# Performance work log

Measured on AMD Instinct MI355X. Metric: run time of the kernel, lower is better.

Reference implementation:

```python
import jax, jax.numpy as jnp
import numpy as np

Nx, Nh, Ny = 512, 512, 2
T, B = 64, 256

def setup_inputs() -> dict:
    key = jax.random.key(0)
    ks = jax.random.split(key, 7)
    x = jax.random.normal(ks[0], (T, B, Nx), dtype=jnp.float32)
    # parameters per random_weight_init([Nx, Nh, Ny], bias=True) + extra W[2]
    w1 = jax.random.normal(ks[1], (Nh, Nx), dtype=jnp.float32) / np.sqrt(Nx)
    b1 = jax.random.normal(ks[2], (Nh, 1), dtype=jnp.float32)
    w2 = (jax.random.normal(ks[3], (Ny, Nh), dtype=jnp.float32) / np.sqrt(Nh)).T  # [Nh, Ny]
    b2 = jax.random.normal(ks[4], (Ny,), dtype=jnp.float32)
    w21 = jax.random.normal(ks[5], (Nh, Ny), dtype=jnp.float32) / np.sqrt(Ny)
    lam = jnp.float32(0.99)
    eta = jnp.float32(-5.0 / Nx)
    return {"x": x, "w1": w1, "b1": b1, "w2": w2, "b2": b2,
            "w21": w21, "lam": lam, "eta": eta}


def reference(x, w1, b1, w2, b2, w21, lam, eta):
    # x: [T, B, Nx]
    lam_c = jnp.minimum(lam, 1.0)  # lam clamped to max=1.0 each forward
    b1v = b1[:, 0]                 # [Nh]

    def step(carry, xt):
        A, a2 = carry              # A: [B, Nh, Nx], a2: [B, Ny]
        # a1 = b1 + (w1 + A) @ x + w21 @ a2
        a1 = (b1v
              + jnp.einsum('hx,bx->bh', w1, xt)
              + jnp.einsum('bhx,bx->bh', A, xt)
              + jnp.einsum('hy,by->bh', w21, a2))
        h = jax.nn.sigmoid(a1)     # [B, Nh]
        # Hebbian fast-weight update: A = lam*A + eta * outer(h, x)
        A_new = lam_c * A + eta * h[:, :, None] * xt[:, None, :]
        a2_new = b2 + h @ w2       # [B, Ny]
        y = jax.nn.sigmoid(a2_new)
        return (A_new, a2_new), (h, y)

    A0 = jnp.zeros((x.shape[1], w1.shape[0], w1.shape[1]), dtype=x.dtype)
    a20 = jnp.zeros((x.shape[1], w2.shape[1]), dtype=x.dtype)
    _, (hiddens, outputs) = jax.lax.scan(step, (A0, a20), x)
    # match torch shapes: hiddens [T, B, Nh, 1], outputs [T, B, Ny]
    return hiddens[..., None], outputs
```

## Files before the change

kernel.cpp:

```cpp
#include <hip/hip_runtime.h>
#include <hip/hip_bf16.h>
#include <math.h>

#define T_STEPS 64
#define BATCH   256
#define NX      512
#define NH      512

typedef short bf16x8 __attribute__((ext_vector_type(8)));
typedef float f32x4  __attribute__((ext_vector_type(4)));

__device__ __forceinline__ float dpp_sum64(float v) {
    v += __int_as_float(__builtin_amdgcn_update_dpp(0, __float_as_int(v), 0x111, 0xf, 0xf, true));
    v += __int_as_float(__builtin_amdgcn_update_dpp(0, __float_as_int(v), 0x112, 0xf, 0xf, true));
    v += __int_as_float(__builtin_amdgcn_update_dpp(0, __float_as_int(v), 0x114, 0xf, 0xf, true));
    v += __int_as_float(__builtin_amdgcn_update_dpp(0, __float_as_int(v), 0x118, 0xf, 0xf, true));
    v += __int_as_float(__builtin_amdgcn_update_dpp(0, __float_as_int(v), 0x142, 0xf, 0xf, true));
    v += __int_as_float(__builtin_amdgcn_update_dpp(0, __float_as_int(v), 0x143, 0xf, 0xf, true));
    return v;
}

__device__ __forceinline__ __hip_bfloat162 cvt2(float a, float b) {
    return __float22bfloat162_rn(make_float2(a, b));
}

__global__ __launch_bounds__(256) void w1_prep_kernel(
    const float* __restrict__ w1, unsigned short* __restrict__ w1f)
{
    int tid = blockIdx.x * 256 + threadIdx.x;
    int row = tid >> 6;
    int oct = tid & 63;
    const float* s = &w1[(size_t)row * 512 + oct * 8];
    float4 v0 = *(const float4*)s;
    float4 v1 = *(const float4*)(s + 4);
    union { __hip_bfloat162 q[4]; int4 pk; } u;
    u.q[0] = cvt2(v0.x, v0.y); u.q[1] = cvt2(v0.z, v0.w);
    u.q[2] = cvt2(v1.x, v1.y); u.q[3] = cvt2(v1.z, v1.w);
    int g = ((oct >> 2) * 32 + (row >> 4)) * 64 + (row & 15) + 16 * (oct & 3);
    *(int4*)&w1f[(size_t)g * 8] = u.pk;
}

__global__ __launch_bounds__(512, 1) void fused_kernel(
    const float* __restrict__ x,
    const unsigned short* __restrict__ w1f,
    const float* __restrict__ b1,
    const float* __restrict__ w2,
    const float* __restrict__ b2,
    const float* __restrict__ w21,
    const float* __restrict__ lamp,
    const float* __restrict__ etap,
    float* __restrict__ outH,
    float* __restrict__ outY)
{
    const int b    = blockIdx.x;
    const int h    = threadIdx.x;
    const int lane = h & 63;
    const int wv   = h >> 6;

    __shared__ float Hs[64][512];
    __shared__ float Gl[64][66];
    __shared__ float C[16][64];
    __shared__ float lam_pow[64];
    __shared__ float red[2][16];

    unsigned short* xs = (unsigned short*)&Hs[0][0];

    const float eta = etap[0];
    const float lam = fminf(lamp[0], 1.0f);
    const float2 w21v = *(const float2*)&w21[2 * h];
    const float2 w2v  = *(const float2*)&w2[2 * h];
    const float b20 = b2[0], b21 = b2[1];
    float* oHb = outH + (size_t)b * NH + h;

    if (h < 64)
        lam_pow[h] = (h == 0) ? 1.0f : exp2f((float)h * log2f(lam));
#pragma unroll
    for (int i = 0; i < 8; ++i) {
        int r = wv + i * 8;
        int o = lane;
        const float* src = &x[((size_t)r * BATCH + b) * NX + o * 8];
        float4 v0 = *(const float4*)src;
        float4 v1 = *(const float4*)(src + 4);
        union { __hip_bfloat162 q[4]; int4 pk; } u;
        u.q[0] = cvt2(v0.x, v0.y); u.q[1] = cvt2(v0.z, v0.w);
        u.q[2] = cvt2(v1.x, v1.y); u.q[3] = cvt2(v1.z, v1.w);
        int g = ((o >> 2) * 4 + (r >> 4)) * 64 + (r & 15) + 16 * (o & 3);
        *(int4*)&xs[g * 8] = u.pk;
    }
    __syncthreads();

    bf16x8 bfp[2][4];
#pragma unroll
    for (int nf = 0; nf < 4; ++nf)
        bfp[0][nf] = *(const bf16x8*)&w1f[(size_t)((wv * 4 + nf) * 64 + lane) * 8];

    {
        const int mt_g = wv >> 1;
#pragma unroll
        for (int j = 0; j < 2; ++j) {
            const int nt_g = (wv & 1) * 2 + j;
            f32x4 gacc = {};
#pragma unroll
            for (int ks = 0; ks < 16; ++ks) {
                bf16x8 afr = *(const bf16x8*)&xs[((ks * 4 + mt_g) * 64 + lane) * 8];
                bf16x8 bfr = *(const bf16x8*)&xs[((ks * 4 + nt_g) * 64 + lane) * 8];
                gacc = __builtin_amdgcn_mfma_f32_16x16x32_bf16(afr, bfr, gacc, 0, 0, 0);
            }
#pragma unroll
            for (int r = 0; r < 4; ++r)
                Gl[mt_g * 16 + ((lane >> 4) << 2) + r][nt_g * 16 + (lane & 15)] = gacc[r];
        }
    }

    {
        f32x4 pacc[4][4] = {};
#pragma unroll
        for (int ks = 0; ks < 16; ++ks) {
            if (ks < 15) {
#pragma unroll
                for (int nf = 0; nf < 4; ++nf)
                    bfp[(ks + 1) & 1][nf] = *(const bf16x8*)
                        &w1f[(size_t)(((ks + 1) * 32 + wv * 4 + nf) * 64 + lane) * 8];
            }
            bf16x8 afr[4];
#pragma unroll
            for (int mt = 0; mt < 4; ++mt)
                afr[mt] = *(const bf16x8*)&xs[((ks * 4 + mt) * 64 + lane) * 8];
#pragma unroll
            for (int mt = 0; mt < 4; ++mt)
#pragma unroll
                for (int nf = 0; nf < 4; ++nf)
                    pacc[mt][nf] = __builtin_amdgcn_mfma_f32_16x16x32_bf16(
                        afr[mt], bfp[ks & 1][nf], pacc[mt][nf], 0, 0, 0);
        }

        __syncthreads();

        float bc[4];
#pragma unroll
        for (int nf = 0; nf < 4; ++nf)
            bc[nf] = b1[wv * 64 + nf * 16 + (lane & 15)];
#pragma unroll
        for (int mt = 0; mt < 4; ++mt) {
#pragma unroll
            for (int nf = 0; nf < 4; ++nf) {
#pragma unroll
                for (int r = 0; r < 4; ++r) {
                    int t = mt * 16 + ((lane >> 4) << 2) + r;
                    int n = wv * 64 + nf * 16 + (lane & 15);
                    Hs[t][n] = pacc[mt][nf][r] + bc[nf];
                }
            }
        }
    }
    __syncthreads();

#pragma unroll 1
    for (int c = 0; c < 4; ++c) {
        const int t0 = c * 16;

#pragma unroll
        for (int e = h; e < 1024; e += 512) {
            int tt = e >> 6, s = e & 63;
            int t  = t0 + tt;
            float cv = 0.f;
            if (s < t) cv = eta * lam_pow[t - 1 - s] * Gl[t][s];
            C[tt][s] = cv;
        }

        float pvreg[16];
#pragma unroll
        for (int tt = 0; tt < 16; ++tt)
            pvreg[tt] = Hs[t0 + tt][h];

        __syncthreads();

        float macc[16] = {};
        for (int s4 = 0; s4 < t0; s4 += 4) {
            float hsv0 = Hs[s4 + 0][h];
            float hsv1 = Hs[s4 + 1][h];
            float hsv2 = Hs[s4 + 2][h];
            float hsv3 = Hs[s4 + 3][h];
#pragma unroll
            for (int tt = 0; tt < 16; ++tt) {
                float4 cf = *(const float4*)&C[tt][s4];
                macc[tt] = fmaf(cf.x, hsv0, macc[tt]);
                macc[tt] = fmaf(cf.y, hsv1, macc[tt]);
                macc[tt] = fmaf(cf.z, hsv2, macc[tt]);
                macc[tt] = fmaf(cf.w, hsv3, macc[tt]);
            }
        }

        float hcur[16];
        float partial = pvreg[0] + macc[0];
#pragma unroll
        for (int tt = 0; tt < 16; ++tt) {
            const int t = t0 + tt;

            float a2x, a2y;
            if (t == 0) {
                a2x = 0.f; a2y = 0.f;
            } else {
                const int pr = (t - 1) & 1;
                float4 r0 = *(const float4*)&red[pr][0];
                float4 r1 = *(const float4*)&red[pr][4];
                float4 r2 = *(const float4*)&red[pr][8];
                float4 r3 = *(const float4*)&red[pr][12];
                float s0 = b20 + ((r0.x + r0.z) + (r1.x + r1.z)) + ((r2.x + r2.z) + (r3.x + r3.z));
                float s1 = b21 + ((r0.y + r0.w) + (r1.y + r1.w)) + ((r2.y + r2.w) + (r3.y + r3.w));
                a2x = s0; a2y = s1;
                if (h == 0) {
                    outY[((size_t)(t - 1) * BATCH + b) * 2 + 0] = 1.0f / (1.0f + __expf(-s0));
                    outY[((size_t)(t - 1) * BATCH + b) * 2 + 1] = 1.0f / (1.0f + __expf(-s1));
                }
            }

            float a1 = partial + w21v.x * a2x + w21v.y * a2y;
            float hv = 1.0f / (1.0f + __expf(-a1));
            hcur[tt] = hv;
            Hs[t][h] = hv;
            oHb[(size_t)t * (BATCH * NH)] = hv;

            float p0 = dpp_sum64(hv * w2v.x);
            float p1 = dpp_sum64(hv * w2v.y);
            if ((h & 63) == 63) {
                red[t & 1][(h >> 6) * 2]     = p0;
                red[t & 1][(h >> 6) * 2 + 1] = p1;
            }

            if (tt < 15) {
                partial = pvreg[tt + 1] + macc[tt + 1];
#pragma unroll
                for (int j = 0; j <= tt; ++j)
                    partial = fmaf(C[tt + 1][t0 + j], hcur[j], partial);
            }

            __syncthreads();
        }
    }

    {
        float4 r0 = *(const float4*)&red[63 & 1][0];
        float4 r1 = *(const float4*)&red[63 & 1][4];
        float4 r2 = *(const float4*)&red[63 & 1][8];
        float4 r3 = *(const float4*)&red[63 & 1][12];
        float s0 = b20 + ((r0.x + r0.z) + (r1.x + r1.z)) + ((r2.x + r2.z) + (r3.x + r3.z));
        float s1 = b21 + ((r0.y + r0.w) + (r1.y + r1.w)) + ((r2.y + r2.w) + (r3.y + r3.w));
        if (h == 0) {
            outY[((size_t)63 * BATCH + b) * 2 + 0] = 1.0f / (1.0f + __expf(-s0));
            outY[((size_t)63 * BATCH + b) * 2 + 1] = 1.0f / (1.0f + __expf(-s1));
        }
    }
}

extern "C" void kernel_launch(void* const* d_in, const int* in_sizes, int n_in,
                              void* d_out, int out_size, void* d_ws, size_t ws_size,
                              hipStream_t stream) {
    const float* x   = (const float*)d_in[0];
    const float* w1  = (const float*)d_in[1];
    const float* b1  = (const float*)d_in[2];
    const float* w2  = (const float*)d_in[3];
    const float* b2  = (const float*)d_in[4];
    const float* w21 = (const float*)d_in[5];
    const float* lam = (const float*)d_in[6];
    const float* eta = (const float*)d_in[7];

    float* outH = (float*)d_out;
    float* outY = outH + (size_t)T_STEPS * BATCH * NH;
    unsigned short* w1f = (unsigned short*)d_ws;

    w1_prep_kernel<<<128, 256, 0, stream>>>(w1, w1f);
    fused_kernel<<<256, 512, 0, stream>>>(x, w1f, b1, w2, b2, w21, lam, eta, outH, outY);
}
```

Measured before the change: 62.42 us.

## Interleave the W1·x projection for the next chunk into the recurrent step loop

The upfront GEMM computing W1·x+b1 for all 64 timesteps is cut down to only the first 16-step chunk. The projection for each following chunk is computed during the serial recurrence of the current chunk: one k-slice of MFMA per step, with x loaded from global memory and converted to bf16 on the fly. This shortens the prologue and hides the projection work inside the latency-bound sequential loop. In exchange, each step gains global loads and MFMAs on its critical path, and 16 fewer accumulator registers are live in the prologue.

```diff
diff --git a/kernel.cpp b/kernel.cpp
--- a/kernel.cpp
+++ b/kernel.cpp
@@ -72,6 +72,11 @@
     const float b20 = b2[0], b21 = b2[1];
     float* oHb = outH + (size_t)b * NH + h;
 
+    float bc[4];
+#pragma unroll
+    for (int nf = 0; nf < 4; ++nf)
+        bc[nf] = b1[wv * 64 + nf * 16 + (lane & 15)];
+
     if (h < 64)
         lam_pow[h] = (h == 0) ? 1.0f : exp2f((float)h * log2f(lam));
 #pragma unroll
@@ -89,11 +94,6 @@
     }
     __syncthreads();
 
-    bf16x8 bfp[2][4];
-#pragma unroll
-    for (int nf = 0; nf < 4; ++nf)
-        bfp[0][nf] = *(const bf16x8*)&w1f[(size_t)((wv * 4 + nf) * 64 + lane) * 8];
-
     {
         const int mt_g = wv >> 1;
 #pragma unroll
@@ -113,45 +113,25 @@
     }
 
     {
-        f32x4 pacc[4][4] = {};
+        f32x4 pacc0[4] = {};
 #pragma unroll
         for (int ks = 0; ks < 16; ++ks) {
-            if (ks < 15) {
-#pragma unroll
-                for (int nf = 0; nf < 4; ++nf)
-                    bfp[(ks + 1) & 1][nf] = *(const bf16x8*)
-                        &w1f[(size_t)(((ks + 1) * 32 + wv * 4 + nf) * 64 + lane) * 8];
-            }
-            bf16x8 afr[4];
-#pragma unroll
-            for (int mt = 0; mt < 4; ++mt)
-                afr[mt] = *(const bf16x8*)&xs[((ks * 4 + mt) * 64 + lane) * 8];
-#pragma unroll
-            for (int mt = 0; mt < 4; ++mt)
-#pragma unroll
-                for (int nf = 0; nf < 4; ++nf)
-                    pacc[mt][nf] = __builtin_amdgcn_mfma_f32_16x16x32_bf16(
-                        afr[mt], bfp[ks & 1][nf], pacc[mt][nf], 0, 0, 0);
-        }
-
+            bf16x8 afr = *(const bf16x8*)&xs[((ks * 4 + 0) * 64 + lane) * 8];
+#pragma unroll
+            for (int nf = 0; nf < 4; ++nf) {
+                bf16x8 bfr = *(const bf16x8*)
+                    &w1f[(size_t)((ks * 32 + wv * 4 + nf) * 64 + lane) * 8];
+                pacc0[nf] = __builtin_amdgcn_mfma_f32_16x16x32_bf16(
+                    afr, bfr, pacc0[nf], 0, 0, 0);
+            }
+        }
         __syncthreads();
-
-        float bc[4];
 #pragma unroll
         for (int nf = 0; nf < 4; ++nf)
-            bc[nf] = b1[wv * 64 + nf * 16 + (lane & 15)];
-#pragma unroll
-        for (int mt = 0; mt < 4; ++mt) {
-#pragma unroll
-            for (int nf = 0; nf < 4; ++nf) {
-#pragma unroll
-                for (int r = 0; r < 4; ++r) {
-                    int t = mt * 16 + ((lane >> 4) << 2) + r;
-                    int n = wv * 64 + nf * 16 + (lane & 15);
-                    Hs[t][n] = pacc[mt][nf][r] + bc[nf];
-                }
-            }
-        }
+#pragma unroll
+            for (int r = 0; r < 4; ++r)
+                Hs[((lane >> 4) << 2) + r][wv * 64 + nf * 16 + (lane & 15)]
+                    = pacc0[nf][r] + bc[nf];
     }
     __syncthreads();
 
@@ -191,6 +171,7 @@
             }
         }
 
+        f32x4 paccN[4] = {};
         float hcur[16];
         float partial = pvreg[0] + macc[0];
 #pragma unroll
@@ -235,6 +216,32 @@
                     partial = fmaf(C[tt + 1][t0 + j], hcur[j], partial);
             }
 
+            if (c < 3) {
+                const float* ax = &x[((size_t)(t0 + 16 + (lane & 15)) * BATCH + b) * NX
+                                     + tt * 32 + (lane >> 4) * 8];
+                float4 a0 = *(const float4*)ax;
+                float4 a1v = *(const float4*)(ax + 4);
+                union { __hip_bfloat162 q[4]; bf16x8 v; } ua;
+                ua.q[0] = cvt2(a0.x, a0.y); ua.q[1] = cvt2(a0.z, a0.w);
+                ua.q[2] = cvt2(a1v.x, a1v.y); ua.q[3] = cvt2(a1v.z, a1v.w);
+#pragma unroll
+                for (int nf = 0; nf < 4; ++nf) {
+                    bf16x8 bfr = *(const bf16x8*)
+                        &w1f[(size_t)((tt * 32 + wv * 4 + nf) * 64 + lane) * 8];
+                    paccN[nf] = __builtin_amdgcn_mfma_f32_16x16x32_bf16(
+                        ua.v, bfr, paccN[nf], 0, 0, 0);
+                }
+                if (tt == 15) {
+#pragma unroll
+                    for (int nf = 0; nf < 4; ++nf)
+#pragma unroll
+                        for (int r = 0; r < 4; ++r)
+                            Hs[t0 + 16 + ((lane >> 4) << 2) + r]
+                              [wv * 64 + nf * 16 + (lane & 15)]
+                                = paccN[nf][r] + bc[nf];
+                }
+            }
+
             __syncthreads();
         }
     }
```

Result: slower. 98.60 us (+58.0%).
